# Kernel optimization log

Hardware: AMD Instinct MI355X
Metric: run time of the kernel (lower is better)

## Reference

```python
import jax, jax.numpy as jnp
import numpy as np

N_NODES = 100000
N_EDGES = 1000000
IN_FEATS = 128
HID_FEATS = 128
OUT_FEATS = 128
N_CLASSES = 16
NEG_SLOPE = 0.01
BN_EPS = 1e-5


def _linear_params(key, d_in, d_out):
    k1, k2 = jax.random.split(key)
    s = 1.0 / np.sqrt(d_in)
    w = jax.random.uniform(k1, (d_in, d_out), jnp.float32, -s, s)
    b = jax.random.uniform(k2, (d_out,), jnp.float32, -s, s)
    return w, b


def setup_inputs() -> dict:
    key = jax.random.key(0)
    ks = jax.random.split(key, 16)
    node_feat = jax.random.normal(ks[0], (N_NODES, IN_FEATS), jnp.float32)
    src = jax.random.randint(ks[1], (N_EDGES,), 0, N_NODES, jnp.int32)
    dst = jax.random.randint(ks[2], (N_EDGES,), 0, N_NODES, jnp.int32)
    dims = [(IN_FEATS, HID_FEATS), (HID_FEATS, HID_FEATS), (HID_FEATS, OUT_FEATS)]
    inp = {"node_feat": node_feat, "src": src, "dst": dst}
    for i, (din, dout) in enumerate(dims):
        wp, bp = _linear_params(ks[3 + 4 * i], din, din)      # fc_pool: d_in -> d_in
        ws, _ = _linear_params(ks[4 + 4 * i], din, dout)       # fc_self (no bias)
        wn, _ = _linear_params(ks[5 + 4 * i], din, dout)       # fc_neigh (no bias)
        _, b = _linear_params(ks[6 + 4 * i], din, dout)        # shared output bias
        inp[f"wp{i}"] = wp; inp[f"bp{i}"] = bp
        inp[f"ws{i}"] = ws; inp[f"wn{i}"] = wn; inp[f"b{i}"] = b
    inp["bn_gamma"] = jnp.ones((HID_FEATS,), jnp.float32)
    inp["bn_beta"] = jnp.zeros((HID_FEATS,), jnp.float32)
    wc, bc = _linear_params(ks[15], OUT_FEATS, N_CLASSES)
    inp["wc"] = wc; inp["bc"] = bc
    return inp


def _sage_pool(h, src, dst, deg_mask, wp, bp, ws, wn, b):
    # fc_pool + relu on source nodes, gather per edge, segment-max to dst
    hp = jax.nn.relu(h @ wp + bp)                 # [N, d_in]
    msg = hp[src]                                 # [E, d_in]
    agg = jax.ops.segment_max(msg, dst, num_segments=N_NODES)  # [N, d_in]
    agg = jnp.where(deg_mask, agg, 0.0)           # zero for isolated nodes
    return h @ ws + agg @ wn + b


def _batchnorm(x, gamma, beta):
    mu = jnp.mean(x, axis=0)
    var = jnp.var(x, axis=0)
    return (x - mu) * jax.lax.rsqrt(var + BN_EPS) * gamma + beta


def reference(node_feat, src, dst,
              wp0, bp0, ws0, wn0, b0,
              wp1, bp1, ws1, wn1, b1,
              wp2, bp2, ws2, wn2, b2,
              bn_gamma, bn_beta, wc, bc):
    deg = jnp.zeros((N_NODES,), jnp.float32).at[dst].add(1.0)
    deg_mask = (deg > 0)[:, None]
    h = jax.nn.leaky_relu(_sage_pool(node_feat, src, dst, deg_mask, wp0, bp0, ws0, wn0, b0), NEG_SLOPE)
    h = jax.nn.leaky_relu(_batchnorm(_sage_pool(h, src, dst, deg_mask, wp1, bp1, ws1, wn1, b1), bn_gamma, bn_beta), NEG_SLOPE)
    h = _sage_pool(h, src, dst, deg_mask, wp2, bp2, ws2, wn2, b2)
    return h @ wc + bc
```

## Files before the change

### kernel.cpp

```cpp
#include <hip/hip_runtime.h>


#define N_NODES 100000
#define N_EDGES 1000000
#define F 128
#define NEG_SLOPE 0.01f
#define BN_EPS 1e-5f
#define NODES_PER_XCD 12500

typedef __attribute__((ext_vector_type(8))) short bf16x8;
typedef __attribute__((ext_vector_type(4))) float f32x4;
typedef __attribute__((ext_vector_type(2))) unsigned short u16x2;

typedef __attribute__((address_space(3))) unsigned int as3_uint;
typedef __attribute__((address_space(1))) const unsigned int as1_cuint;

__device__ __forceinline__ void gload16(const void* g, void* l) {
    __builtin_amdgcn_global_load_lds((as1_cuint*)g, (as3_uint*)l, 16, 0, 0);
}

__device__ __forceinline__ unsigned short f2bf(float f) {
    unsigned int u = __float_as_uint(f);
    u += 0x7fff + ((u >> 16) & 1);
    return (unsigned short)(u >> 16);
}
__device__ __forceinline__ float bf2f(unsigned short h) {
    return __uint_as_float(((unsigned int)h) << 16);
}

__global__ __launch_bounds__(256) void zero_misc_kernel(
    float4* __restrict__ deg4, float4* __restrict__ stats4)
{
    if (blockIdx.x < 98) {
        const int i = blockIdx.x * 256 + threadIdx.x;
        if (i < 25000) deg4[i] = make_float4(0.f, 0.f, 0.f, 0.f);
    } else {
        if (threadIdx.x < 64) stats4[threadIdx.x] = make_float4(0.f, 0.f, 0.f, 0.f);
    }
}

#define PREP_GROUPS 4483
__global__ __launch_bounds__(256) void prep_kernel(
    const float4* __restrict__ nf, uint2* __restrict__ xout,
    const int* __restrict__ dst, int* __restrict__ deg,
    const float* __restrict__ w0, const float* __restrict__ w1, const float* __restrict__ w2,
    const float* __restrict__ w3, const float* __restrict__ w4, const float* __restrict__ w5,
    const float* __restrict__ w6, const float* __restrict__ w7, const float* __restrict__ w8,
    short* __restrict__ wp_p, short* __restrict__ wsn_p)
{
    const int g = blockIdx.x >> 2;
    const int k = blockIdx.x & 3;
    const int tid = threadIdx.x;
    if (k < 3) {
        const int c = g * 3 + k;
        if (c >= 12500) return;
        const long i = (long)c * 256 + tid;
        float4 v = nf[i];
        uint2 o;
        o.x = (unsigned)f2bf(v.x) | ((unsigned)f2bf(v.y) << 16);
        o.y = (unsigned)f2bf(v.z) | ((unsigned)f2bf(v.w) << 16);
        xout[i] = o;
        return;
    }
    if (g < 3907) {
        const int e = g * 256 + tid;
        if (e < N_EDGES) atomicAdd(&deg[__builtin_nontemporal_load(&dst[e])], 1);
        return;
    }
    const int po = g - 3907;
    if (po >= 576) return;
    const int idx = po * 256 + tid;
    const int matid = idx >> 14;
    const int layer = (matid * 11) >> 5;
    const int mat = matid - 3 * layer;
    const int i = idx & 16383;
    const int kk = i >> 7, n = i & 127;
    const float* srcm;
    switch (matid) {
        case 0: srcm = w0; break; case 1: srcm = w1; break; case 2: srcm = w2; break;
        case 3: srcm = w3; break; case 4: srcm = w4; break; case 5: srcm = w5; break;
        case 6: srcm = w6; break; case 7: srcm = w7; break; default: srcm = w8; break;
    }
    const int slot = ((kk >> 3) * 128 + n) * 8 + (kk & 7);
    const short v = (short)f2bf(srcm[i]);
    if (mat == 0) wp_p[layer * 16384 + slot] = v;
    else wsn_p[layer * 32768 + (mat == 2 ? 16384 : 0) + slot] = v;
}

template<int NKS>
__device__ __forceinline__ void gemm_body(
    const int bid,
    const short* __restrict__ A1, const short* __restrict__ A2,
    const short* __restrict__ Bp, const float* __restrict__ bias,
    unsigned short* __restrict__ Cout, const int n_rows, const int act)
{
    constexpr int S = NKS / 2;
    __shared__ short tile[2 * 8192];

    const int tid = threadIdx.x;
    const int wave = tid >> 6;
    const int lane = tid & 63;
    const int m = lane & 15, q = lane >> 4;
    const int r0 = bid * 128;
    const int rw = (wave >> 1) * 64;
    const int r0q = r0 + rw;
    const int c0 = (wave & 1) * 64;
    const int gchunk = (tid & 7) ^ ((tid >> 3) & 7);

    f32x4 acc[4][4];
#pragma unroll
    for (int i = 0; i < 4; ++i)
#pragma unroll
        for (int j = 0; j < 4; ++j)
#pragma unroll
            for (int r = 0; r < 4; ++r) acc[i][j][r] = 0.f;

    auto stage = [&](int s, int buf) {
        const short* Ap = (NKS == 8 && s >= 2) ? A2 : A1;
        const int kbase = (s & 1) * 64;
#pragma unroll
        for (int p = 0; p < 4; ++p) {
            int row = r0 + (tid >> 3) + 32 * p;
            row = min(row, n_rows - 1);
            gload16(Ap + (size_t)row * F + kbase + gchunk * 8,
                    &tile[buf * 8192 + p * 2048 + tid * 8]);
        }
    };

    stage(0, 0);
    __syncthreads();

    for (int s = 0; s < S; ++s) {
        if (s + 1 < S) stage(s + 1, (s + 1) & 1);
        const short* tb = &tile[(s & 1) * 8192];
#pragma unroll
        for (int ks2 = 0; ks2 < 2; ++ks2) {
            const int ks32 = s * 2 + ks2;
            bf16x8 b[4], a[4];
#pragma unroll
            for (int ni = 0; ni < 4; ++ni)
                b[ni] = *(const bf16x8*)(Bp + ((size_t)(ks32 * 4 + q) * F + c0 + ni * 16 + m) * 8);
#pragma unroll
            for (int mi = 0; mi < 4; ++mi)
                a[mi] = *(const bf16x8*)(tb + (rw + mi * 16 + m) * 64 + (((ks2 * 4 + q) ^ (m & 7)) << 3));
#pragma unroll
            for (int mi = 0; mi < 4; ++mi)
#pragma unroll
                for (int ni = 0; ni < 4; ++ni)
                    acc[mi][ni] = __builtin_amdgcn_mfma_f32_16x16x32_bf16(a[mi], b[ni], acc[mi][ni], 0, 0, 0);
        }
        __syncthreads();
    }

    float bv[4];
#pragma unroll
    for (int ni = 0; ni < 4; ++ni) bv[ni] = bias[c0 + ni * 16 + m];

    short* ep = &tile[wave * 1280];
    const int colc_lo = m >> 3, cin = m & 7;
#pragma unroll
    for (int mi = 0; mi < 4; ++mi) {
#pragma unroll
        for (int ni = 0; ni < 4; ++ni) {
            const int colc = 2 * ni + colc_lo;
#pragma unroll
            for (int rg = 0; rg < 4; ++rg) {
                const int row16 = q * 4 + rg;
                float v = acc[mi][ni][rg] + bv[ni];
                if (act == 1) v = v > 0.f ? v : 0.f;
                else if (act == 2) v = v > 0.f ? v : v * NEG_SLOPE;
                ep[row16 * 80 + ((colc ^ (row16 & 7)) << 3) + cin] = (short)f2bf(v);
            }
        }
        __syncthreads();
#pragma unroll
        for (int p = 0; p < 2; ++p) {
            const int lrow = (lane >> 3) + 8 * p;
            bf16x8 vv = *(const bf16x8*)&ep[lrow * 80 + (((lane & 7) ^ (lrow & 7)) << 3)];
            const int grow = r0q + mi * 16 + lrow;
            if (grow < n_rows)
                *(bf16x8*)(Cout + (size_t)grow * F + c0 + ((lane & 7) << 3)) = vv;
        }
        __syncthreads();
    }
}

template<int NKS>
__global__ __launch_bounds__(256) void gemm_mfma(
    const short* __restrict__ A1, const short* __restrict__ A2,
    const short* __restrict__ Bp, const float* __restrict__ bias,
    unsigned short* __restrict__ Cout, int n_rows, int act)
{
    gemm_body<NKS>(blockIdx.x, A1, A2, Bp, bias, Cout, n_rows, act);
}

__global__ __launch_bounds__(256) void scan1_kernel(const int* __restrict__ deg, int* __restrict__ bsum) {
    __shared__ int sh[256];
    const int t = threadIdx.x;
    const int base = blockIdx.x * 1024 + t * 4;
    int s = 0;
#pragma unroll
    for (int j = 0; j < 4; ++j) s += (base + j < N_NODES) ? deg[base + j] : 0;
    sh[t] = s; __syncthreads();
    for (int off = 128; off; off >>= 1) {
        if (t < off) sh[t] += sh[t + off];
        __syncthreads();
    }
    if (t == 0) bsum[blockIdx.x] = sh[0];
}

__global__ __launch_bounds__(128) void scan2_kernel(int* __restrict__ bsum, int nb, int* __restrict__ row_start) {
    __shared__ int sh[128];
    const int t = threadIdx.x;
    sh[t] = (t < nb) ? bsum[t] : 0;
    __syncthreads();
    for (int off = 1; off < 128; off <<= 1) {
        int x = (t >= off) ? sh[t - off] : 0;
        __syncthreads();
        if (t >= off) sh[t] += x;
        __syncthreads();
    }
    if (t < nb) bsum[t] = t ? sh[t - 1] : 0;
    if (t == 0) row_start[N_NODES] = N_EDGES;
}

__global__ __launch_bounds__(256) void scan3_kernel(
    const int* __restrict__ deg, const int* __restrict__ boff,
    int* __restrict__ row_start, int* __restrict__ cursor)
{
    __shared__ int sh[256];
    const int t = threadIdx.x;
    const int base = blockIdx.x * 1024 + t * 4;
    int v[4]; int s = 0;
#pragma unroll
    for (int j = 0; j < 4; ++j) { v[j] = (base + j < N_NODES) ? deg[base + j] : 0; s += v[j]; }
    sh[t] = s; __syncthreads();
    for (int off = 1; off < 256; off <<= 1) {
        int x = (t >= off) ? sh[t - off] : 0;
        __syncthreads();
        if (t >= off) sh[t] += x;
        __syncthreads();
    }
    int excl = (t ? sh[t - 1] : 0) + boff[blockIdx.x];
#pragma unroll
    for (int j = 0; j < 4; ++j) {
        if (base + j < N_NODES) { row_start[base + j] = excl; cursor[base + j] = excl; }
        excl += v[j];
    }
}

__global__ __launch_bounds__(256) void scatter_gemm_kernel(
    const int* __restrict__ src, const int* __restrict__ dst,
    int* __restrict__ cursor, int* __restrict__ esrc,
    const short* __restrict__ A1, const short* __restrict__ Bp,
    const float* __restrict__ bias, unsigned short* __restrict__ Cout)
{
    const int bid = blockIdx.x;
    const int grp = bid >> 3;
    const int t8 = bid & 7;
    const int sgrp = grp / 7;
    const int u = grp - sgrp * 7;
    if (u < 5) {
        const int lo = t8 * NODES_PER_XCD;
        const int chunk = sgrp * 5 + u;
        const int e0 = chunk * 4096 + threadIdx.x;
        int d[16]; bool hit[16];
#pragma unroll
        for (int j = 0; j < 16; ++j) {
            const int e = e0 + j * 256;
            d[j] = dst[min(e, N_EDGES - 1)];
        }
#pragma unroll
        for (int j = 0; j < 16; ++j)
            hit[j] = (e0 + j * 256 < N_EDGES) & ((unsigned)(d[j] - lo) < (unsigned)NODES_PER_XCD);
        int sv[16];
#pragma unroll
        for (int j = 0; j < 16; ++j)
            if (hit[j]) sv[j] = src[e0 + j * 256];
        int pos[16];
#pragma unroll
        for (int j = 0; j < 16; ++j)
            if (hit[j]) pos[j] = atomicAdd(&cursor[d[j]], 1);
#pragma unroll
        for (int j = 0; j < 16; ++j)
            if (hit[j]) esrc[pos[j]] = sv[j];
    } else {
        const int g = (sgrp * 2 + (u - 5)) * 8 + t8;
        if (g >= (N_NODES + 127) / 128) return;
        gemm_body<4>(g, A1, (const short*)nullptr, Bp, bias, Cout, N_NODES, 1);
    }
}

__global__ __launch_bounds__(256) void aggregate_max_bf16(
    const unsigned int* __restrict__ hp, const int* __restrict__ row_start,
    const int* __restrict__ esrc, unsigned int* __restrict__ agg)
{
    const int node = blockIdx.x * 4 + (threadIdx.x >> 6);
    if (node >= N_NODES) return;
    const int lane = threadIdx.x & 63;
    const int beg = row_start[node], end = row_start[node + 1];
    u16x2 mm = (u16x2)0;
    for (int base = beg; base < end; base += 16) {
        int s[16];
#pragma unroll
        for (int j = 0; j < 16; ++j) {
            const int t = base + j;
            s[j] = esrc[(t < end) ? t : beg];
        }
        unsigned int v[16];
#pragma unroll
        for (int j = 0; j < 16; ++j) v[j] = hp[(size_t)s[j] * 64 + lane];
#pragma unroll
        for (int j = 0; j < 16; ++j)
            mm = __builtin_elementwise_max(mm, __builtin_bit_cast(u16x2, v[j]));
    }
    agg[(size_t)node * 64 + lane] = __builtin_bit_cast(unsigned int, mm);
}

#define BN_ROWS_PER_BLOCK 196
__global__ __launch_bounds__(256) void bn_stats_kernel(
    const unsigned short* __restrict__ x, float* __restrict__ stats, int n)
{
    const int tid = threadIdx.x;
    const int wave = tid >> 6, lane = tid & 63;
    const int rgrp = lane >> 4;
    const int c16 = lane & 15;
    const int rbase = blockIdx.x * BN_ROWS_PER_BLOCK;
    const int rend = min(rbase + BN_ROWS_PER_BLOCK, n);

    float s[8], ss[8];
#pragma unroll
    for (int j = 0; j < 8; ++j) { s[j] = 0.f; ss[j] = 0.f; }

    for (int r = rbase + wave * 4 + rgrp; r < rend; r += 16) {
        const uint4 v = *(const uint4*)(x + (size_t)r * F + c16 * 8);
        const unsigned int w[4] = {v.x, v.y, v.z, v.w};
#pragma unroll
        for (int u = 0; u < 4; ++u) {
            const float f0 = bf2f((unsigned short)(w[u] & 0xffffu));
            const float f1 = bf2f((unsigned short)(w[u] >> 16));
            s[2*u]   += f0; ss[2*u]   = fmaf(f0, f0, ss[2*u]);
            s[2*u+1] += f1; ss[2*u+1] = fmaf(f1, f1, ss[2*u+1]);
        }
    }
#pragma unroll
    for (int j = 0; j < 8; ++j) {
        s[j]  += __shfl_down(s[j], 32);  s[j]  += __shfl_down(s[j], 16);
        ss[j] += __shfl_down(ss[j], 32); ss[j] += __shfl_down(ss[j], 16);
    }
    __shared__ float sh[4][16][16];
    if (lane < 16) {
#pragma unroll
        for (int j = 0; j < 8; ++j) {
            sh[wave][c16][2*j]     = s[j];
            sh[wave][c16][2*j + 1] = ss[j];
        }
    }
    __syncthreads();
    const float tot = sh[0][tid >> 4][tid & 15] + sh[1][tid >> 4][tid & 15]
                    + sh[2][tid >> 4][tid & 15] + sh[3][tid >> 4][tid & 15];
    const int col = (tid >> 4) * 8 + ((tid >> 1) & 7);
    atomicAdd(&stats[(tid & 1) * 128 + col], tot);
}

__global__ void bn_finalize_kernel(
    const float* __restrict__ stats, const float* __restrict__ gamma,
    const float* __restrict__ beta, float* __restrict__ coef)
{
    const int c = threadIdx.x;
    const float mean = stats[c] * (1.f / N_NODES);
    const float var = stats[128 + c] * (1.f / N_NODES) - mean * mean;
    const float scale = gamma[c] * rsqrtf(var + BN_EPS);
    coef[c] = scale;
    coef[128 + c] = fmaf(-mean, scale, beta[c]);
}

__global__ __launch_bounds__(256) void bn_apply_bf16(
    unsigned int* __restrict__ x, const float* __restrict__ coef, long n2)
{
    __shared__ float sc[128], sf[128];
    if (threadIdx.x < 128) {
        sc[threadIdx.x] = coef[threadIdx.x];
        sf[threadIdx.x] = coef[128 + threadIdx.x];
    }
    __syncthreads();
    const long i = (long)blockIdx.x * 256 + threadIdx.x;
    if (i >= n2) return;
    const unsigned int v = x[i];
    const int c0 = (int)(i & 63) * 2;
    float a = fmaf(bf2f((unsigned short)(v & 0xffffu)), sc[c0], sf[c0]);
    float b = fmaf(bf2f((unsigned short)(v >> 16)), sc[c0 + 1], sf[c0 + 1]);
    a = a > 0.f ? a : a * NEG_SLOPE;
    b = b > 0.f ? b : b * NEG_SLOPE;
    x[i] = (unsigned)f2bf(a) | ((unsigned)f2bf(b) << 16);
}

__global__ __launch_bounds__(256) void classifier_kernel(
    const unsigned short* __restrict__ X, const float* __restrict__ Wc,
    const float* __restrict__ bc, float* __restrict__ out, int n)
{
    __shared__ float Wl[2048];
    __shared__ float Xs[16 * 132];
    const int tid = threadIdx.x;
    for (int i = tid; i < 2048; i += 256) Wl[i] = Wc[i];
    const int r0 = blockIdx.x * 16;
    for (int i = tid; i < 2048; i += 256) {
        const int row = i >> 7, col = i & 127;
        const int gr = r0 + row;
        Xs[row * 132 + col] = (gr < n) ? bf2f(X[(size_t)gr * F + col]) : 0.f;
    }
    __syncthreads();
    const int rl = tid >> 4, c = tid & 15;
    const int r = r0 + rl;
    if (r >= n) return;
    float s = bc[c];
    const float* xr = &Xs[rl * 132];
#pragma unroll
    for (int k = 0; k < 128; ++k) s = fmaf(xr[k], Wl[k * 16 + c], s);
    out[(size_t)r * 16 + c] = s;
}

extern "C" void kernel_launch(void* const* d_in, const int* in_sizes, int n_in,
                              void* d_out, int out_size, void* d_ws, size_t ws_size,
                              hipStream_t stream) {
    const float* node_feat = (const float*)d_in[0];
    const int* src = (const int*)d_in[1];
    const int* dst = (const int*)d_in[2];
    const float* wp[3] = {(const float*)d_in[3],  (const float*)d_in[8],  (const float*)d_in[13]};
    const float* bp[3] = {(const float*)d_in[4],  (const float*)d_in[9],  (const float*)d_in[14]};
    const float* wsm[3] = {(const float*)d_in[5], (const float*)d_in[10], (const float*)d_in[15]};
    const float* wn[3] = {(const float*)d_in[6],  (const float*)d_in[11], (const float*)d_in[16]};
    const float* bb[3] = {(const float*)d_in[7],  (const float*)d_in[12], (const float*)d_in[17]};
    const float* gamma = (const float*)d_in[18];
    const float* beta  = (const float*)d_in[19];
    const float* wc    = (const float*)d_in[20];
    const float* bc    = (const float*)d_in[21];

    const size_t SZ = (size_t)N_NODES * F;
    short* sbase = (short*)d_ws;
    short* B0  = sbase;
    short* B1  = sbase + SZ;
    short* B2  = sbase + 2 * SZ;
    short* Xbf = sbase + 3 * SZ;
    short* wp_p  = sbase + 4 * SZ;
    short* wsn_p = wp_p + 3 * 16384;
    float* fbase = (float*)(wsn_p + 3 * 32768);
    float* stats = fbase;
    float* coef  = fbase + 256;
    int* ibase = (int*)(fbase + 512);
    int* deg       = ibase;
    int* row_start = ibase + 100000;
    int* cursor    = ibase + 200104;
    int* esrc      = ibase + 300104;
    int* bsum      = ibase + 1300104;

    const int gGemm = (N_NODES + 127) / 128;
    const int gScan = (N_NODES + 1023) / 1024;
    const int gAgg  = (N_NODES + 3) / 4;
    const long n2   = (long)(SZ / 2);

    zero_misc_kernel<<<99, 256, 0, stream>>>((float4*)deg, (float4*)stats);

    prep_kernel<<<PREP_GROUPS * 4, 256, 0, stream>>>(
        (const float4*)node_feat, (uint2*)Xbf, dst, deg,
        wp[0], wsm[0], wn[0], wp[1], wsm[1], wn[1], wp[2], wsm[2], wn[2],
        wp_p, wsn_p);

    scan1_kernel<<<gScan, 256, 0, stream>>>(deg, bsum);
    scan2_kernel<<<1, 128, 0, stream>>>(bsum, gScan, row_start);
    scan3_kernel<<<gScan, 256, 0, stream>>>(deg, bsum, row_start, cursor);

    scatter_gemm_kernel<<<2744, 256, 0, stream>>>(
        src, dst, cursor, esrc,
        Xbf, wp_p, bp[0], (unsigned short*)B0);

    const short* Xl[3]  = {Xbf, B0, B1};
    short* hpb[3]       = {B0, B1, B0};
    short* aggb[3]      = {B1, B2, B2};
    short* Yb[3]        = {B0, B1, B0};
    for (int l = 0; l < 3; ++l) {
        const short* X = Xl[l];
        if (l > 0)
            gemm_mfma<4><<<gGemm, 256, 0, stream>>>(X, (const short*)nullptr,
                wp_p + l * 16384, bp[l], (unsigned short*)hpb[l], N_NODES, 1);
        aggregate_max_bf16<<<gAgg, 256, 0, stream>>>(
            (const unsigned int*)hpb[l], row_start, esrc, (unsigned int*)aggb[l]);
        const int act = (l == 0) ? 2 : 0;
        gemm_mfma<8><<<gGemm, 256, 0, stream>>>(X, aggb[l],
            wsn_p + l * 32768, bb[l], (unsigned short*)Yb[l], N_NODES, act);
        if (l == 1) {
            bn_stats_kernel<<<512, 256, 0, stream>>>(
                (const unsigned short*)Yb[l], stats, N_NODES);
            bn_finalize_kernel<<<1, 128, 0, stream>>>(stats, gamma, beta, coef);
            bn_apply_bf16<<<(int)((n2 + 255) / 256), 256, 0, stream>>>(
                (unsigned int*)Yb[l], coef, n2);
        }
    }
    classifier_kernel<<<(N_NODES + 15) / 16, 256, 0, stream>>>(
        (const unsigned short*)B0, wc, bc, (float*)d_out, N_NODES);
}
```

Before: 529.2 us.

## Fuse segment-max neighbor gather into the self/neighbor GEMM kernel

Removes the standalone aggregate_max kernel. Each GEMM block now gathers the max-aggregated neighbor features for its 128 rows into registers and stages them into shared memory as the second half of the K dimension. This avoids writing the aggregation buffer to global memory and reading it back, and cuts kernel launches per layer. The trade-off is far fewer waves doing the irregular gather, serial per-node loops per wave, and higher register pressure, which may expose gather latency.

```diff
diff --git a/kernel.cpp b/kernel.cpp
--- a/kernel.cpp
+++ b/kernel.cpp
@@ -194,6 +194,149 @@
     gemm_body<NKS>(blockIdx.x, A1, A2, Bp, bias, Cout, n_rows, act);
 }
 
+__global__ __launch_bounds__(256) void gather_gemm8(
+    const short* __restrict__ A1, const unsigned int* __restrict__ hp,
+    const int* __restrict__ row_start, const int* __restrict__ esrc,
+    const short* __restrict__ Bp, const float* __restrict__ bias,
+    unsigned short* __restrict__ Cout, int n_rows, int act)
+{
+    __shared__ short tile[2 * 8192];
+
+    const int tid = threadIdx.x;
+    const int wave = tid >> 6;
+    const int lane = tid & 63;
+    const int m = lane & 15, q = lane >> 4;
+    const int r0 = blockIdx.x * 128;
+    const int rw = (wave >> 1) * 64;
+    const int r0q = r0 + rw;
+    const int c0 = (wave & 1) * 64;
+    const int gchunk = (tid & 7) ^ ((tid >> 3) & 7);
+
+    unsigned int aggv[32];
+    {
+        const int nb = r0 + wave * 32;
+#pragma unroll
+        for (int j = 0; j < 32; ++j) {
+            const int n = min(nb + j, N_NODES - 1);
+            const int beg = row_start[n], end = row_start[n + 1];
+            u16x2 mm = (u16x2)0;
+            for (int base = beg; base < end; base += 16) {
+                int s[16];
+#pragma unroll
+                for (int t = 0; t < 16; ++t) {
+                    const int e = base + t;
+                    s[t] = esrc[(e < end) ? e : beg];
+                }
+#pragma unroll
+                for (int t = 0; t < 16; ++t) {
+                    const unsigned int v = hp[(size_t)s[t] * 64 + lane];
+                    mm = __builtin_elementwise_max(mm, __builtin_bit_cast(u16x2, v));
+                }
+            }
+            aggv[j] = __builtin_bit_cast(unsigned int, mm);
+        }
+    }
+
+    f32x4 acc[4][4];
+#pragma unroll
+    for (int i = 0; i < 4; ++i)
+#pragma unroll
+        for (int j = 0; j < 4; ++j)
+#pragma unroll
+            for (int r = 0; r < 4; ++r) acc[i][j][r] = 0.f;
+
+    auto stageX = [&](int s, int buf) {
+        const int kbase = s * 64;
+#pragma unroll
+        for (int p = 0; p < 4; ++p) {
+            int row = r0 + (tid >> 3) + 32 * p;
+            row = min(row, n_rows - 1);
+            gload16(A1 + (size_t)row * F + kbase + gchunk * 8,
+                    &tile[buf * 8192 + p * 2048 + tid * 8]);
+        }
+    };
+
+    auto write_agg_half = [&](int h) {
+        if ((lane >> 5) == h) {
+            const int cb = (2 * lane) & 63;
+            const int c = cb >> 3;
+            const int ci = (cb & 7) >> 1;
+            unsigned int* lt = (unsigned int*)&tile[h * 8192];
+#pragma unroll
+            for (int j = 0; j < 32; ++j) {
+                const int r = wave * 32 + j;
+                lt[r * 32 + ((c ^ (r & 7)) << 2) + ci] = aggv[j];
+            }
+        }
+    };
+
+    auto compute_step = [&](int s) {
+        const short* tb = &tile[(s & 1) * 8192];
+#pragma unroll
+        for (int ks2 = 0; ks2 < 2; ++ks2) {
+            const int ks32 = s * 2 + ks2;
+            bf16x8 b[4], a[4];
+#pragma unroll
+            for (int ni = 0; ni < 4; ++ni)
+                b[ni] = *(const bf16x8*)(Bp + ((size_t)(ks32 * 4 + q) * F + c0 + ni * 16 + m) * 8);
+#pragma unroll
+            for (int mi = 0; mi < 4; ++mi)
+                a[mi] = *(const bf16x8*)(tb + (rw + mi * 16 + m) * 64 + (((ks2 * 4 + q) ^ (m & 7)) << 3));
+#pragma unroll
+            for (int mi = 0; mi < 4; ++mi)
+#pragma unroll
+                for (int ni = 0; ni < 4; ++ni)
+                    acc[mi][ni] = __builtin_amdgcn_mfma_f32_16x16x32_bf16(a[mi], b[ni], acc[mi][ni], 0, 0, 0);
+        }
+    };
+
+    stageX(0, 0);
+    __syncthreads();
+    stageX(1, 1);
+    compute_step(0);
+    __syncthreads();
+    write_agg_half(0);
+    compute_step(1);
+    __syncthreads();
+    write_agg_half(1);
+    compute_step(2);
+    __syncthreads();
+    compute_step(3);
+    __syncthreads();
+
+    float bv[4];
+#pragma unroll
+    for (int ni = 0; ni < 4; ++ni) bv[ni] = bias[c0 + ni * 16 + m];
+
+    short* ep = &tile[wave * 1280];
+    const int colc_lo = m >> 3, cin = m & 7;
+#pragma unroll
+    for (int mi = 0; mi < 4; ++mi) {
+#pragma unroll
+        for (int ni = 0; ni < 4; ++ni) {
+            const int colc = 2 * ni + colc_lo;
+#pragma unroll
+            for (int rg = 0; rg < 4; ++rg) {
+                const int row16 = q * 4 + rg;
+                float v = acc[mi][ni][rg] + bv[ni];
+                if (act == 1) v = v > 0.f ? v : 0.f;
+                else if (act == 2) v = v > 0.f ? v : v * NEG_SLOPE;
+                ep[row16 * 80 + ((colc ^ (row16 & 7)) << 3) + cin] = (short)f2bf(v);
+            }
+        }
+        __syncthreads();
+#pragma unroll
+        for (int p = 0; p < 2; ++p) {
+            const int lrow = (lane >> 3) + 8 * p;
+            bf16x8 vv = *(const bf16x8*)&ep[lrow * 80 + (((lane & 7) ^ (lrow & 7)) << 3)];
+            const int grow = r0q + mi * 16 + lrow;
+            if (grow < n_rows)
+                *(bf16x8*)(Cout + (size_t)grow * F + c0 + ((lane & 7) << 3)) = vv;
+        }
+        __syncthreads();
+    }
+}
+
 __global__ __launch_bounds__(256) void scan1_kernel(const int* __restrict__ deg, int* __restrict__ bsum) {
     __shared__ int sh[256];
     const int t = threadIdx.x;
@@ -289,32 +432,6 @@
         if (g >= (N_NODES + 127) / 128) return;
         gemm_body<4>(g, A1, (const short*)nullptr, Bp, bias, Cout, N_NODES, 1);
     }
-}
-
-__global__ __launch_bounds__(256) void aggregate_max_bf16(
-    const unsigned int* __restrict__ hp, const int* __restrict__ row_start,
-    const int* __restrict__ esrc, unsigned int* __restrict__ agg)
-{
-    const int node = blockIdx.x * 4 + (threadIdx.x >> 6);
-    if (node >= N_NODES) return;
-    const int lane = threadIdx.x & 63;
-    const int beg = row_start[node], end = row_start[node + 1];
-    u16x2 mm = (u16x2)0;
-    for (int base = beg; base < end; base += 16) {
-        int s[16];
-#pragma unroll
-        for (int j = 0; j < 16; ++j) {
-            const int t = base + j;
-            s[j] = esrc[(t < end) ? t : beg];
-        }
-        unsigned int v[16];
-#pragma unroll
-        for (int j = 0; j < 16; ++j) v[j] = hp[(size_t)s[j] * 64 + lane];
-#pragma unroll
-        for (int j = 0; j < 16; ++j)
-            mm = __builtin_elementwise_max(mm, __builtin_bit_cast(u16x2, v[j]));
-    }
-    agg[(size_t)node * 64 + lane] = __builtin_bit_cast(unsigned int, mm);
 }
 
 #define BN_ROWS_PER_BLOCK 196
@@ -456,7 +573,6 @@
 
     const int gGemm = (N_NODES + 127) / 128;
     const int gScan = (N_NODES + 1023) / 1024;
-    const int gAgg  = (N_NODES + 3) / 4;
     const long n2   = (long)(SZ / 2);
 
     zero_misc_kernel<<<99, 256, 0, stream>>>((float4*)deg, (float4*)stats);
@@ -474,28 +590,28 @@
         src, dst, cursor, esrc,
         Xbf, wp_p, bp[0], (unsigned short*)B0);
 
-    const short* Xl[3]  = {Xbf, B0, B1};
-    short* hpb[3]       = {B0, B1, B0};
-    short* aggb[3]      = {B1, B2, B2};
-    short* Yb[3]        = {B0, B1, B0};
-    for (int l = 0; l < 3; ++l) {
-        const short* X = Xl[l];
-        if (l > 0)
-            gemm_mfma<4><<<gGemm, 256, 0, stream>>>(X, (const short*)nullptr,
-                wp_p + l * 16384, bp[l], (unsigned short*)hpb[l], N_NODES, 1);
-        aggregate_max_bf16<<<gAgg, 256, 0, stream>>>(
-            (const unsigned int*)hpb[l], row_start, esrc, (unsigned int*)aggb[l]);
-        const int act = (l == 0) ? 2 : 0;
-        gemm_mfma<8><<<gGemm, 256, 0, stream>>>(X, aggb[l],
-            wsn_p + l * 32768, bb[l], (unsigned short*)Yb[l], N_NODES, act);
-        if (l == 1) {
-            bn_stats_kernel<<<512, 256, 0, stream>>>(
-                (const unsigned short*)Yb[l], stats, N_NODES);
-            bn_finalize_kernel<<<1, 128, 0, stream>>>(stats, gamma, beta, coef);
-            bn_apply_bf16<<<(int)((n2 + 255) / 256), 256, 0, stream>>>(
-                (unsigned int*)Yb[l], coef, n2);
-        }
-    }
+    gather_gemm8<<<gGemm, 256, 0, stream>>>(
+        Xbf, (const unsigned int*)B0, row_start, esrc,
+        wsn_p, bb[0], (unsigned short*)B1, N_NODES, 2);
+
+    gemm_mfma<4><<<gGemm, 256, 0, stream>>>(B1, (const short*)nullptr,
+        wp_p + 16384, bp[1], (unsigned short*)B0, N_NODES, 1);
+    gather_gemm8<<<gGemm, 256, 0, stream>>>(
+        B1, (const unsigned int*)B0, row_start, esrc,
+        wsn_p + 32768, bb[1], (unsigned short*)B2, N_NODES, 0);
+
+    bn_stats_kernel<<<512, 256, 0, stream>>>(
+        (const unsigned short*)B2, stats, N_NODES);
+    bn_finalize_kernel<<<1, 128, 0, stream>>>(stats, gamma, beta, coef);
+    bn_apply_bf16<<<(int)((n2 + 255) / 256), 256, 0, stream>>>(
+        (unsigned int*)B2, coef, n2);
+
+    gemm_mfma<4><<<gGemm, 256, 0, stream>>>(B2, (const short*)nullptr,
+        wp_p + 2 * 16384, bp[2], (unsigned short*)B0, N_NODES, 1);
+    gather_gemm8<<<gGemm, 256, 0, stream>>>(
+        B2, (const unsigned int*)B0, row_start, esrc,
+        wsn_p + 2 * 32768, bb[2], (unsigned short*)B1, N_NODES, 0);
+
     classifier_kernel<<<(N_NODES + 15) / 16, 256, 0, stream>>>(
-        (const unsigned short*)B0, wc, bc, (float*)d_out, N_NODES);
-}
+        (const unsigned short*)B1, wc, bc, (float*)d_out, N_NODES);
+}
```

Measured after the change: 637.6 us. +20.5%, slower.
